# Optimization experiments

Hardware: AMD Instinct MI355X
Metric: run time of the kernel (lower is better)

The kernel has to match this reference:

```python
import jax, jax.numpy as jnp
import numpy as np

B, N, DIM, H = 64, 196, 1024, 32
HD = DIM // H  # 32, must equal H for the bias broadcast quirk
S = 14  # sqrt(num_patches)


def _relative_position_index(s):
    coords = np.stack(np.meshgrid(np.arange(s), np.arange(s), indexing='ij'))  # [2,s,s]
    cf = coords.reshape(2, -1)  # [2, N]
    rel = (cf[:, :, None] - cf[:, None, :]).transpose(1, 2, 0)  # [N,N,2]
    rel[..., 0] += s - 1
    rel[..., 1] += s - 1
    rel[..., 0] *= 2 * s - 1
    return rel.sum(-1).astype(np.int32)  # [N,N], values in [0, (2s-1)^2)


def setup_inputs() -> dict:
    key = jax.random.key(0)
    k0, k1, k2, k3 = jax.random.split(key, 4)
    x = jax.random.normal(k0, (B, N, DIM), dtype=jnp.float32)
    W_qkv = jax.random.normal(k1, (DIM, 3 * DIM), dtype=jnp.float32) * 0.02
    W_proj = jax.random.normal(k2, (DIM, DIM), dtype=jnp.float32) * 0.02
    b_proj = jnp.zeros((DIM,), dtype=jnp.float32)
    rpk = jax.random.normal(k3, ((2 * S - 1) ** 2, HD), dtype=jnp.float32)  # [729, HD]
    rel_idx = jnp.asarray(_relative_position_index(S))  # [N, N] int32
    return {"x": x, "W_qkv": W_qkv, "W_proj": W_proj, "b_proj": b_proj,
            "rpk": rpk, "rel_idx": rel_idx}


def reference(x, W_qkv, W_proj, b_proj, rpk, rel_idx):
    b, n, c = x.shape
    scale = HD ** -0.5
    qkv = (x @ W_qkv).reshape(b, n, 3, H, HD)  # [B,N,3,H,HD]
    q, k, v = jnp.moveaxis(qkv, 2, 0)          # each [B,N,H,HD]
    q = q.transpose(0, 2, 1, 3)                # [B,H,N,HD]
    k = k.transpose(0, 2, 1, 3)
    v = v.transpose(0, 2, 1, 3)
    attn = jnp.einsum('bhnd,bhmd->bhnm', q, k) * scale  # [B,H,N,N]
    # gather relative-position bias: [N*N, HD] -> [N,N,HD] -> [HD,N,N]
    bias = rpk[rel_idx.reshape(-1)].reshape(n, n, HD).transpose(2, 0, 1)
    attn = jax.nn.softmax(attn + bias[None], axis=-1)   # bias broadcasts since HD == H
    out = jnp.einsum('bhnm,bhmd->bhnd', attn, v)        # [B,H,N,HD]
    out = out.transpose(0, 2, 1, 3).reshape(b, n, c)    # [B,N,C]
    return out @ W_proj + b_proj
```

## Files before the change

### kernel.cpp

```cpp
#include <hip/hip_runtime.h>
#include <hip/hip_bf16.h>

typedef __bf16 bf16_t;
typedef __attribute__((ext_vector_type(8))) __bf16 bf16x8;
typedef __attribute__((ext_vector_type(4))) __bf16 bf16x4;
typedef __attribute__((ext_vector_type(4))) float f32x4;

#define NPOS 38416
#define NPAD 224
#define KSTR 40
#define VSTR 232

__device__ __forceinline__ void async_copy16(const bf16_t* g, bf16_t* l) {
  __builtin_amdgcn_global_load_lds((const __attribute__((address_space(1))) void*)g,
                                   (__attribute__((address_space(3))) void*)l, 16, 0, 0);
}

__global__ __launch_bounds__(256) void cast_x_kernel(const float* __restrict__ x,
                                                     bf16_t* __restrict__ xb, int n4) {
  int i = blockIdx.x * 256 + threadIdx.x;
  if (i < n4) {
    float4 v = ((const float4*)x)[i];
    bf16x4 o;
    o[0] = (bf16_t)v.x; o[1] = (bf16_t)v.y; o[2] = (bf16_t)v.z; o[3] = (bf16_t)v.w;
    ((bf16x4*)xb)[i] = o;
  }
}

__global__ __launch_bounds__(256) void transpose_cast_kernel(const float* __restrict__ src,
                                                             bf16_t* __restrict__ dst,
                                                             int K, int Ncols) {
  __shared__ float tile[32][33];
  int t = threadIdx.x;
  int tx = t & 31, ty = t >> 5;
  int bx = blockIdx.x, by = blockIdx.y;
  for (int r = ty; r < 32; r += 8)
    tile[r][tx] = src[(size_t)(by * 32 + r) * Ncols + bx * 32 + tx];
  __syncthreads();
  for (int r = ty; r < 32; r += 8)
    dst[(size_t)(bx * 32 + r) * K + by * 32 + tx] = (bf16_t)tile[tx][r];
}

__global__ __launch_bounds__(256) void bias_gather_kernel(const float* __restrict__ rpk,
                                                          const int* __restrict__ rel_idx,
                                                          float* __restrict__ bias) {
  int pos = blockIdx.x * 256 + threadIdx.x;
  if (pos < NPOS) {
    int idx = rel_idx[pos];
    const float* r = rpk + idx * 32;
#pragma unroll
    for (int h = 0; h < 32; ++h) bias[h * NPOS + pos] = r[h];
  }
}

template <int MODE>
__global__ __launch_bounds__(512, 4) void gemm_bt_kernel(
    const bf16_t* __restrict__ A, const bf16_t* __restrict__ Bt,
    bf16_t* __restrict__ qo, bf16_t* __restrict__ ko, bf16_t* __restrict__ vto,
    float* __restrict__ fo, const float* __restrict__ bp) {
  constexpr int K = 1024;
  constexpr int CH = 384 * 32;
  __shared__ alignas(16) bf16_t S[2][CH];
  const int t = threadIdx.x;
  const int lane = t & 63;
  const int quad = lane >> 4;
  const int l16 = lane & 15;
  const int wave = t >> 6;
  const int m0 = blockIdx.y * 256, n0 = blockIdx.x * 128;
  const int wr = (wave >> 1) * 64, wc = (wave & 1) * 64;

  const bf16_t* gp[3];
  int lofs[3];
#pragma unroll
  for (int j = 0; j < 3; ++j) {
    const int c = t + j * 512;
    const int row = c >> 2;
    const int sc = (c & 3) ^ ((c >> 3) & 3);
    gp[j] = (row < 256) ? A + (size_t)(m0 + row) * K + sc * 8
                        : Bt + (size_t)(n0 + row - 256) * K + sc * 8;
    lofs[j] = c * 8;
  }

  const int qa = quad ^ ((l16 >> 1) & 3);

  const f32x4 vzero = {0.f, 0.f, 0.f, 0.f};
  f32x4 acc[4][4];
#pragma unroll
  for (int i = 0; i < 4; ++i)
#pragma unroll
    for (int j = 0; j < 4; ++j) acc[i][j] = vzero;

#pragma unroll
  for (int j = 0; j < 3; ++j) async_copy16(gp[j], &S[0][lofs[j]]);

  for (int it = 0; it < K / 32; ++it) {
    __syncthreads();
    const bf16_t* Sb = S[it & 1];
    if (it + 1 < K / 32) {
      bf16_t* Sn = S[(it + 1) & 1];
      const int kt = (it + 1) * 32;
#pragma unroll
      for (int j = 0; j < 3; ++j) async_copy16(gp[j] + kt, Sn + lofs[j]);
    }
    const bf16_t* As = Sb;
    const bf16_t* Bs = Sb + 256 * 32;
    bf16x8 af[4], bfr[4];
#pragma unroll
    for (int i = 0; i < 4; ++i) {
      af[i] = *(const bf16x8*)(As + (wr + i * 16 + l16) * 32 + qa * 8);
      bfr[i] = *(const bf16x8*)(Bs + (wc + i * 16 + l16) * 32 + qa * 8);
    }
#pragma unroll
    for (int i = 0; i < 4; ++i)
#pragma unroll
      for (int j = 0; j < 4; ++j)
        acc[i][j] = __builtin_amdgcn_mfma_f32_16x16x32_bf16(af[i], bfr[j], acc[i][j], 0, 0, 0);
  }

  if (MODE == 0) {
    const float qscale = 0.17677669529663687f;
    const int which = n0 >> 10;
#pragma unroll
    for (int i = 0; i < 4; ++i) {
      const int rb = m0 + wr + i * 16 + quad * 4;
#pragma unroll
      for (int j = 0; j < 4; ++j) {
        const int c = n0 + wc + j * 16 + l16;
        const int h = (c >> 5) & 31, d = c & 31;
#pragma unroll
        for (int r = 0; r < 4; ++r) {
          const int rg = rb + r;
          const int b = rg / 196, n = rg - b * 196;
          const float v = acc[i][j][r];
          if (which == 0)
            qo[(((size_t)b * 32 + h) * 196 + n) * 32 + d] = (bf16_t)(v * qscale);
          else if (which == 1)
            ko[(((size_t)b * 32 + h) * 196 + n) * 32 + d] = (bf16_t)v;
          else
            vto[(((size_t)b * 32 + h) * 32 + d) * 196 + n] = (bf16_t)v;
        }
      }
    }
  } else {
#pragma unroll
    for (int i = 0; i < 4; ++i) {
      const int rb = m0 + wr + i * 16 + quad * 4;
#pragma unroll
      for (int j = 0; j < 4; ++j) {
        const int c = n0 + wc + j * 16 + l16;
        const float bias_c = bp[c];
#pragma unroll
        for (int r = 0; r < 4; ++r)
          fo[(size_t)(rb + r) * 1024 + c] = acc[i][j][r] + bias_c;
      }
    }
  }
}

__global__ __launch_bounds__(256, 2) void attn_kernel(
    const bf16_t* __restrict__ q, const bf16_t* __restrict__ kmat,
    const bf16_t* __restrict__ vtg, const float* __restrict__ bias,
    bf16_t* __restrict__ attn_out) {
  __shared__ alignas(16) bf16_t kf[NPAD * KSTR];
  __shared__ alignas(16) bf16_t vts[32 * VSTR];
  __shared__ alignas(16) bf16_t pb[4][16 * VSTR];

  const int t = threadIdx.x;
  const int lane = t & 63;
  const int quad = lane >> 4, l16 = lane & 15;
  const int wave = t >> 6;
  const int bh = blockIdx.x;
  const int b = bh >> 5, h = bh & 31;
  const bf16_t* qg = q + (size_t)bh * (196 * 32);
  const bf16_t* kg = kmat + (size_t)bh * (196 * 32);
  const bf16_t* vg = vtg + (size_t)bh * (32 * 196);
  const float* bg = bias + (size_t)h * NPOS;

  {
    const uint4* src = (const uint4*)kg;
    uint4* dst = (uint4*)kf;
    for (int c = t; c < 784; c += 256) dst[(c >> 2) * 5 + (c & 3)] = src[c];
    const uint4 z4 = {0u, 0u, 0u, 0u};
    if (t < 112) {
      int r = 196 + (t >> 2), ch = t & 3;
      dst[r * 5 + ch] = z4;
    }
    const uint2 z2 = {0u, 0u};
    for (int i = t; i < 1792; i += 256) {
      int d = i / 56, c = i - d * 56;
      uint2 val = (c < 49) ? ((const uint2*)(vg + d * 196))[c] : z2;
      ((uint2*)(vts + d * VSTR))[c] = val;
    }
  }
  __syncthreads();

  const f32x4 vzero = {0.f, 0.f, 0.f, 0.f};
  bf16_t* pw = &pb[wave][0];

  for (int ch = wave; ch < 13; ch += 4) {
    const int q0 = ch * 16;
    int qrow = q0 + l16;
    if (qrow > 195) qrow = 195;
    const bf16x8 aq = *(const bf16x8*)(qg + qrow * 32 + quad * 8);

    float bv[13][4];
#pragma unroll
    for (int ct = 0; ct < 13; ++ct) {
      const int col = ct * 16 + l16;
#pragma unroll
      for (int r = 0; r < 4; ++r) {
        int br = q0 + quad * 4 + r;
        if (br > 195) br = 195;
        bv[ct][r] = (col < 196) ? bg[br * 196 + col] : 0.f;
      }
    }

    f32x4 s[13];
#pragma unroll
    for (int ct = 0; ct < 13; ++ct) {
      const bf16x8 bk = *(const bf16x8*)(kf + (ct * 16 + l16) * KSTR + quad * 8);
      s[ct] = __builtin_amdgcn_mfma_f32_16x16x32_bf16(aq, bk, vzero, 0, 0, 0);
    }
#pragma unroll
    for (int ct = 0; ct < 13; ++ct) {
      const int col = ct * 16 + l16;
#pragma unroll
      for (int r = 0; r < 4; ++r) {
        if (col < 196)
          s[ct][r] += bv[ct][r];
        else
          s[ct][r] = -1e30f;
      }
    }
    float mx[4], inv[4];
#pragma unroll
    for (int r = 0; r < 4; ++r) {
      float m = s[0][r];
#pragma unroll
      for (int ct = 1; ct < 13; ++ct) m = fmaxf(m, s[ct][r]);
      m = fmaxf(m, __shfl_xor(m, 1));
      m = fmaxf(m, __shfl_xor(m, 2));
      m = fmaxf(m, __shfl_xor(m, 4));
      m = fmaxf(m, __shfl_xor(m, 8));
      mx[r] = m;
    }
#pragma unroll
    for (int ct = 0; ct < 13; ++ct)
#pragma unroll
      for (int r = 0; r < 4; ++r) s[ct][r] = __expf(s[ct][r] - mx[r]);
#pragma unroll
    for (int r = 0; r < 4; ++r) {
      float sum = s[0][r];
#pragma unroll
      for (int ct = 1; ct < 13; ++ct) sum += s[ct][r];
      sum += __shfl_xor(sum, 1);
      sum += __shfl_xor(sum, 2);
      sum += __shfl_xor(sum, 4);
      sum += __shfl_xor(sum, 8);
      inv[r] = 1.f / sum;
    }
#pragma unroll
    for (int ct = 0; ct < 13; ++ct) {
      const int col = ct * 16 + l16;
#pragma unroll
      for (int r = 0; r < 4; ++r) pw[(quad * 4 + r) * VSTR + col] = (bf16_t)s[ct][r];
    }
    if (lane < 32) {
      const bf16x8 z8 = {};
      *(bf16x8*)(pw + (lane >> 1) * VSTR + 208 + (lane & 1) * 8) = z8;
    }
#pragma unroll
    for (int dt = 0; dt < 2; ++dt) {
      f32x4 o = vzero;
#pragma unroll
      for (int kk = 0; kk < 7; ++kk) {
        const bf16x8 ap = *(const bf16x8*)(pw + l16 * VSTR + kk * 32 + quad * 8);
        const bf16x8 bv2 = *(const bf16x8*)(vts + (dt * 16 + l16) * VSTR + kk * 32 + quad * 8);
        o = __builtin_amdgcn_mfma_f32_16x16x32_bf16(ap, bv2, o, 0, 0, 0);
      }
      const int d = dt * 16 + l16;
#pragma unroll
      for (int r = 0; r < 4; ++r) {
        const int n = q0 + quad * 4 + r;
        if (n < 196)
          attn_out[(((size_t)b * 196 + n) * 32 + h) * 32 + d] = (bf16_t)(o[r] * inv[r]);
      }
    }
  }
}

extern "C" void kernel_launch(void* const* d_in, const int* in_sizes, int n_in,
                              void* d_out, int out_size, void* d_ws, size_t ws_size,
                              hipStream_t stream) {
  (void)in_sizes; (void)n_in; (void)out_size; (void)ws_size;
  const float* x = (const float*)d_in[0];
  const float* Wqkv = (const float*)d_in[1];
  const float* Wproj = (const float*)d_in[2];
  const float* bproj = (const float*)d_in[3];
  const float* rpk = (const float*)d_in[4];
  const int* rel_idx = (const int*)d_in[5];
  float* out = (float*)d_out;

  char* ws = (char*)d_ws;
  bf16_t* xb = (bf16_t*)(ws + 0);
  bf16_t* wqkvT = (bf16_t*)(ws + 25690112);
  bf16_t* wprojT = (bf16_t*)(ws + 31981568);
  bf16_t* q = (bf16_t*)(ws + 34078720);
  bf16_t* kk = (bf16_t*)(ws + 59768832);
  bf16_t* vt = (bf16_t*)(ws + 85458944);
  float* bias = (float*)(ws + 111149056);
  bf16_t* attn = xb;

  cast_x_kernel<<<12544, 256, 0, stream>>>(x, xb, 12845056 / 4);
  transpose_cast_kernel<<<dim3(96, 32), 256, 0, stream>>>(Wqkv, wqkvT, 1024, 3072);
  transpose_cast_kernel<<<dim3(32, 32), 256, 0, stream>>>(Wproj, wprojT, 1024, 1024);
  bias_gather_kernel<<<151, 256, 0, stream>>>(rpk, rel_idx, bias);
  gemm_bt_kernel<0><<<dim3(24, 49), 512, 0, stream>>>(xb, wqkvT, q, kk, vt, nullptr, nullptr);
  attn_kernel<<<2048, 256, 0, stream>>>(q, kk, vt, bias, attn);
  gemm_bt_kernel<1><<<dim3(8, 49), 512, 0, stream>>>(attn, wprojT, nullptr, nullptr, nullptr, out, bproj);
}
```

Measured before the change: 342.6 us.

## Enlarge GEMM tiles to 256x256 with a four-stage async LDS pipeline

Reworks the bf16 MFMA GEMM used for the QKV and output projections. Block tiles grow from 256x128 to 256x256, so each wave computes 128x64 with 32 accumulators. The shared-memory double buffer becomes a 4-deep ring filled by global_load_lds, using explicit vmcnt waits, barriers, sched_barrier and setprio around the MFMA burst. LDS layout changes to contiguous 16-row panels without the XOR swizzle. This targets load latency and global traffic per FLOP. The cost is more registers and LDS (occupancy 2), half as many blocks, and a possible rise in LDS bank conflicts.

```diff
diff --git a/kernel.cpp b/kernel.cpp
--- a/kernel.cpp
+++ b/kernel.cpp
@@ -53,75 +53,86 @@
   }
 }
 
+#define GSTAGE(KT)                                                            \
+  do {                                                                        \
+    _Pragma("unroll") for (int _j = 0; _j < 4; ++_j)                          \
+        async_copy16(gp[_j] + (KT) * 32, &Sh[(KT) & 3][lofs[_j]]);            \
+  } while (0)
+
+#define KSTEP(IT, VN)                                                         \
+  do {                                                                        \
+    __builtin_amdgcn_sched_barrier(0);                                        \
+    asm volatile("s_waitcnt vmcnt(" VN ")" ::: "memory");                     \
+    __builtin_amdgcn_s_barrier();                                             \
+    __builtin_amdgcn_sched_barrier(0);                                        \
+    const bf16_t* Sb = &Sh[(IT) & 3][0];                                      \
+    bf16x8 af[8], bfr[4];                                                     \
+    _Pragma("unroll") for (int _i = 0; _i < 8; ++_i)                          \
+        af[_i] = *(const bf16x8*)(Sb + (wrp + _i) * 512 + qoff);              \
+    _Pragma("unroll") for (int _j = 0; _j < 4; ++_j)                          \
+        bfr[_j] = *(const bf16x8*)(Sb + 8192 + (wcp + _j) * 512 + qoff);      \
+    __builtin_amdgcn_s_setprio(1);                                            \
+    _Pragma("unroll") for (int _i = 0; _i < 8; ++_i)                          \
+        _Pragma("unroll") for (int _j = 0; _j < 4; ++_j)                      \
+            acc[_i][_j] = __builtin_amdgcn_mfma_f32_16x16x32_bf16(            \
+                af[_i], bfr[_j], acc[_i][_j], 0, 0, 0);                       \
+    __builtin_amdgcn_s_setprio(0);                                            \
+    __builtin_amdgcn_sched_barrier(0);                                        \
+    __builtin_amdgcn_s_barrier();                                             \
+  } while (0)
+
 template <int MODE>
-__global__ __launch_bounds__(512, 4) void gemm_bt_kernel(
+__global__ __launch_bounds__(512, 2) void gemm_bt_kernel(
     const bf16_t* __restrict__ A, const bf16_t* __restrict__ Bt,
     bf16_t* __restrict__ qo, bf16_t* __restrict__ ko, bf16_t* __restrict__ vto,
     float* __restrict__ fo, const float* __restrict__ bp) {
   constexpr int K = 1024;
-  constexpr int CH = 384 * 32;
-  __shared__ alignas(16) bf16_t S[2][CH];
+  __shared__ alignas(16) bf16_t Sh[4][16384];
   const int t = threadIdx.x;
   const int lane = t & 63;
   const int quad = lane >> 4;
   const int l16 = lane & 15;
   const int wave = t >> 6;
-  const int m0 = blockIdx.y * 256, n0 = blockIdx.x * 128;
-  const int wr = (wave >> 1) * 64, wc = (wave & 1) * 64;
-
-  const bf16_t* gp[3];
-  int lofs[3];
-#pragma unroll
-  for (int j = 0; j < 3; ++j) {
-    const int c = t + j * 512;
-    const int row = c >> 2;
-    const int sc = (c & 3) ^ ((c >> 3) & 3);
-    gp[j] = (row < 256) ? A + (size_t)(m0 + row) * K + sc * 8
-                        : Bt + (size_t)(n0 + row - 256) * K + sc * 8;
-    lofs[j] = c * 8;
-  }
-
-  const int qa = quad ^ ((l16 >> 1) & 3);
+  const int m0 = blockIdx.y * 256, n0 = blockIdx.x * 256;
+  const int wr = (wave >> 2) * 128, wc = (wave & 3) * 64;
+  const int wrp = wr >> 4, wcp = wc >> 4;
+  const int qoff = quad * 128 + l16 * 8;
+
+  const bf16_t* gp[4];
+  int lofs[4];
+#pragma unroll
+  for (int j = 0; j < 4; ++j) {
+    const int p = wave * 4 + j;
+    const int pr = (p < 16 ? p : p - 16) * 16 + l16;
+    gp[j] = (p < 16) ? A + (size_t)(m0 + pr) * K + quad * 8
+                     : Bt + (size_t)(n0 + pr) * K + quad * 8;
+    lofs[j] = p * 512 + lane * 8;
+  }
 
   const f32x4 vzero = {0.f, 0.f, 0.f, 0.f};
-  f32x4 acc[4][4];
-#pragma unroll
-  for (int i = 0; i < 4; ++i)
+  f32x4 acc[8][4];
+#pragma unroll
+  for (int i = 0; i < 8; ++i)
 #pragma unroll
     for (int j = 0; j < 4; ++j) acc[i][j] = vzero;
 
-#pragma unroll
-  for (int j = 0; j < 3; ++j) async_copy16(gp[j], &S[0][lofs[j]]);
-
-  for (int it = 0; it < K / 32; ++it) {
-    __syncthreads();
-    const bf16_t* Sb = S[it & 1];
-    if (it + 1 < K / 32) {
-      bf16_t* Sn = S[(it + 1) & 1];
-      const int kt = (it + 1) * 32;
-#pragma unroll
-      for (int j = 0; j < 3; ++j) async_copy16(gp[j] + kt, Sn + lofs[j]);
-    }
-    const bf16_t* As = Sb;
-    const bf16_t* Bs = Sb + 256 * 32;
-    bf16x8 af[4], bfr[4];
-#pragma unroll
-    for (int i = 0; i < 4; ++i) {
-      af[i] = *(const bf16x8*)(As + (wr + i * 16 + l16) * 32 + qa * 8);
-      bfr[i] = *(const bf16x8*)(Bs + (wc + i * 16 + l16) * 32 + qa * 8);
-    }
-#pragma unroll
-    for (int i = 0; i < 4; ++i)
-#pragma unroll
-      for (int j = 0; j < 4; ++j)
-        acc[i][j] = __builtin_amdgcn_mfma_f32_16x16x32_bf16(af[i], bfr[j], acc[i][j], 0, 0, 0);
-  }
+  GSTAGE(0);
+  GSTAGE(1);
+  GSTAGE(2);
+
+  for (int it = 0; it < 29; ++it) {
+    GSTAGE(it + 3);
+    KSTEP(it, "12");
+  }
+  KSTEP(29, "8");
+  KSTEP(30, "4");
+  KSTEP(31, "0");
 
   if (MODE == 0) {
     const float qscale = 0.17677669529663687f;
     const int which = n0 >> 10;
 #pragma unroll
-    for (int i = 0; i < 4; ++i) {
+    for (int i = 0; i < 8; ++i) {
       const int rb = m0 + wr + i * 16 + quad * 4;
 #pragma unroll
       for (int j = 0; j < 4; ++j) {
@@ -143,7 +154,7 @@
     }
   } else {
 #pragma unroll
-    for (int i = 0; i < 4; ++i) {
+    for (int i = 0; i < 8; ++i) {
       const int rb = m0 + wr + i * 16 + quad * 4;
 #pragma unroll
       for (int j = 0; j < 4; ++j) {
@@ -315,7 +326,7 @@
   transpose_cast_kernel<<<dim3(96, 32), 256, 0, stream>>>(Wqkv, wqkvT, 1024, 3072);
   transpose_cast_kernel<<<dim3(32, 32), 256, 0, stream>>>(Wproj, wprojT, 1024, 1024);
   bias_gather_kernel<<<151, 256, 0, stream>>>(rpk, rel_idx, bias);
-  gemm_bt_kernel<0><<<dim3(24, 49), 512, 0, stream>>>(xb, wqkvT, q, kk, vt, nullptr, nullptr);
+  gemm_bt_kernel<0><<<dim3(12, 49), 512, 0, stream>>>(xb, wqkvT, q, kk, vt, nullptr, nullptr);
   attn_kernel<<<2048, 256, 0, stream>>>(q, kk, vt, bias, attn);
-  gemm_bt_kernel<1><<<dim3(8, 49), 512, 0, stream>>>(attn, wprojT, nullptr, nullptr, nullptr, out, bproj);
-}
+  gemm_bt_kernel<1><<<dim3(4, 49), 512, 0, stream>>>(attn, wprojT, nullptr, nullptr, nullptr, out, bproj);
+}
```

Measured after the change: 377.2 us. 1.1x slower.
